# Performance work log

Measured on AMD Instinct MI355X. Metric: run time of the kernel, lower is better.

Reference implementation:

```python
import jax, jax.numpy as jnp
import numpy as np

N, E = 50000, 800000
IN, HID, H, C = 128, 64, 4, 2
NEG_SLOPE = 0.2


def _gat_layer(h, src, dst, W, al, ar, b, out_dim, residual, resW=None, act='elu'):
    # h: [N, in]; W: [H*out, in]; al/ar: [H, out]; b: [H*out]
    n = h.shape[0]
    feat = (h @ W.T).reshape(n, H, out_dim)            # [N, H, out]
    el = jnp.einsum('nho,ho->nh', feat, al)            # [N, H]
    er = jnp.einsum('nho,ho->nh', feat, ar)            # [N, H]
    e = jax.nn.leaky_relu(el[src] + er[dst], NEG_SLOPE)  # [E, H]
    # segment softmax over incoming edges of each dst node
    emax = jax.ops.segment_max(e, dst, num_segments=n)
    ee = jnp.exp(e - emax[dst])
    denom = jax.ops.segment_sum(ee, dst, num_segments=n)
    alpha = ee / denom[dst]                             # [E, H]
    msg = feat[src] * alpha[:, :, None]                 # [E, H, out]
    rst = jax.ops.segment_sum(msg, dst, num_segments=n)  # [N, H, out]
    if residual == 'id':
        rst = rst + h.reshape(n, H, out_dim)
    elif residual == 'fc':
        rst = rst + (h @ resW.T).reshape(n, H, out_dim)
    rst = rst + b.reshape(1, H, out_dim)
    if act == 'elu':
        rst = jax.nn.elu(rst)
    else:  # softmax over last dim (F.softmax)
        rst = jax.nn.softmax(rst, axis=-1)
    return rst


def setup_inputs() -> dict:
    key = jax.random.key(0)
    ks = jax.random.split(key, 24)
    x = jax.random.normal(ks[0], (N, IN), dtype=jnp.float32)
    src = jax.random.randint(ks[1], (E,), 0, N)
    dst = jax.random.randint(ks[2], (E,), 0, N)
    s = 0.1
    d = {'x': x, 'src': src, 'dst': dst}
    # layer 1: IN -> (H, HID), no residual
    d['W1'] = jax.random.normal(ks[3], (H * HID, IN), dtype=jnp.float32) * s
    d['al1'] = jax.random.normal(ks[4], (H, HID), dtype=jnp.float32) * s
    d['ar1'] = jax.random.normal(ks[5], (H, HID), dtype=jnp.float32) * s
    d['b1'] = jnp.zeros((H * HID,), dtype=jnp.float32)
    # layers 2,3: H*HID -> (H, HID), identity residual
    d['W2'] = jax.random.normal(ks[6], (H * HID, H * HID), dtype=jnp.float32) * s
    d['al2'] = jax.random.normal(ks[7], (H, HID), dtype=jnp.float32) * s
    d['ar2'] = jax.random.normal(ks[8], (H, HID), dtype=jnp.float32) * s
    d['b2'] = jnp.zeros((H * HID,), dtype=jnp.float32)
    d['W3'] = jax.random.normal(ks[9], (H * HID, H * HID), dtype=jnp.float32) * s
    d['al3'] = jax.random.normal(ks[10], (H, HID), dtype=jnp.float32) * s
    d['ar3'] = jax.random.normal(ks[11], (H, HID), dtype=jnp.float32) * s
    d['b3'] = jnp.zeros((H * HID,), dtype=jnp.float32)
    # layer 4: H*HID -> (H, C), linear residual, softmax activation, mean over heads
    d['W4'] = jax.random.normal(ks[12], (H * C, H * HID), dtype=jnp.float32) * s
    d['al4'] = jax.random.normal(ks[13], (H, C), dtype=jnp.float32) * s
    d['ar4'] = jax.random.normal(ks[14], (H, C), dtype=jnp.float32) * s
    d['b4'] = jnp.zeros((H * C,), dtype=jnp.float32)
    d['resW4'] = jax.random.normal(ks[15], (H * C, H * HID), dtype=jnp.float32) * s
    return d


def reference(x, src, dst, W1, al1, ar1, b1, W2, al2, ar2, b2, W3, al3, ar3, b3, W4, al4, ar4, b4, resW4):
    h = _gat_layer(x, src, dst, W1, al1, ar1, b1, HID, 'none', act='elu').reshape(N, H * HID)
    h = _gat_layer(h, src, dst, W2, al2, ar2, b2, HID, 'id', act='elu').reshape(N, H * HID)
    h = _gat_layer(h, src, dst, W3, al3, ar3, b3, HID, 'id', act='elu').reshape(N, H * HID)
    h = _gat_layer(h, src, dst, W4, al4, ar4, b4, C, 'fc', resW=resW4, act='softmax')
    return h.mean(axis=1)  # [N, C]
```

## Files before the change

### kernel.cpp

```cpp
#include <hip/hip_runtime.h>
#include <hip/hip_bf16.h>
#include <math.h>


#define LEAKY_SLOPE 0.2f

typedef __bf16 bf16x8_t __attribute__((ext_vector_type(8)));
typedef float f32x4_t __attribute__((ext_vector_type(4)));

__device__ __forceinline__ float leaky(float x) { return x > 0.f ? x : LEAKY_SLOPE * x; }
__device__ __forceinline__ float eluf(float x)  { return x > 0.f ? x : expm1f(x); }
__device__ __forceinline__ float bflo(unsigned u) { return __uint_as_float(u << 16); }
__device__ __forceinline__ float bfhi(unsigned u) { return __uint_as_float(u & 0xffff0000u); }

__device__ __forceinline__ int rli(int v, int l) { return __builtin_amdgcn_readlane(v, l); }
__device__ __forceinline__ float rlf(float v, int l) {
  return __uint_as_float((unsigned)__builtin_amdgcn_readlane((int)__float_as_uint(v), l));
}
template <int CTRL>
__device__ __forceinline__ float dpp_add(float x) {
  int t = __builtin_amdgcn_update_dpp(0, (int)__float_as_uint(x), CTRL, 0xf, 0xf, false);
  return x + __uint_as_float((unsigned)t);
}
__device__ __forceinline__ float wsum_dpp(float x) {
  x = dpp_add<0x111>(x);
  x = dpp_add<0x112>(x);
  x = dpp_add<0x114>(x);
  x = dpp_add<0x118>(x);
  x = dpp_add<0x142>(x);
  x = dpp_add<0x143>(x);
  return rlf(x, 63);
}
__device__ __forceinline__ float wmax(float v) {
#pragma unroll
  for (int o = 32; o; o >>= 1) v = fmaxf(v, __shfl_xor(v, o));
  return v;
}
__device__ __forceinline__ float wsum_sh(float v) {
#pragma unroll
  for (int o = 32; o; o >>= 1) v += __shfl_xor(v, o);
  return v;
}

__device__ __forceinline__ void gl_lds16(const __hip_bfloat16* g, __bf16* l) {
  __builtin_amdgcn_global_load_lds((const __attribute__((address_space(1))) void*)g,
                                   (__attribute__((address_space(3))) void*)l, 16, 0, 0);
}

__global__ void hist_k(const int* __restrict__ dst, int* __restrict__ deg, int e) {
  int i = blockIdx.x * 256 + threadIdx.x;
  if (i < e) atomicAdd(&deg[dst[i]], 1);
}

__global__ __launch_bounds__(1024) void scan1_k(const int* __restrict__ deg,
                                                int* __restrict__ rowp,
                                                int* __restrict__ bsum, int n) {
  __shared__ int sd[1024];
  int tid = threadIdx.x;
  int i = blockIdx.x * 1024 + tid;
  int v = (i < n) ? deg[i] : 0;
  int x = v;
  sd[tid] = x;
  __syncthreads();
  for (int off = 1; off < 1024; off <<= 1) {
    int t = (tid >= off) ? sd[tid - off] : 0;
    __syncthreads();
    x += t;
    sd[tid] = x;
    __syncthreads();
  }
  if (i < n) rowp[i] = x - v;
  if (tid == 1023) bsum[blockIdx.x] = x;
}

__global__ __launch_bounds__(64) void scan2_k(int* __restrict__ bsum, int nb) {
  int lane = threadIdx.x;
  if (nb <= 64) {
    int v = (lane < nb) ? bsum[lane] : 0;
    int x = v;
#pragma unroll
    for (int off = 1; off < 64; off <<= 1) {
      int t = __shfl_up(x, off);
      if (lane >= off) x += t;
    }
    if (lane < nb) bsum[lane] = x - v;
    if (lane == 63) bsum[nb] = x;
  } else if (lane == 0) {
    int run = 0;
    for (int i = 0; i < nb; ++i) { int t = bsum[i]; bsum[i] = run; run += t; }
    bsum[nb] = run;
  }
}

__global__ void scan3_k(const int* __restrict__ bsum, int* __restrict__ rowp, int n, int nb) {
  int i = blockIdx.x * 256 + threadIdx.x;
  if (i < n) rowp[i] += bsum[i >> 10];
  if (i == n) rowp[n] = bsum[nb];
}

__global__ void scatter_k(const int* __restrict__ src, const int* __restrict__ dst,
                          const int* __restrict__ rowp, int* __restrict__ cur,
                          int* __restrict__ csrc, int e) {
  int i = blockIdx.x * 256 + threadIdx.x;
  if (i < e) {
    int d = dst[i];
    int p = atomicAdd(&cur[d], 1);
    csrc[rowp[d] + p] = src[i];
  }
}

__global__ void cvtall_k(const float* __restrict__ x, const float* __restrict__ W1,
                         const float* __restrict__ W2, const float* __restrict__ W3,
                         const float* __restrict__ W4, const float* __restrict__ rW4,
                         __hip_bfloat16* __restrict__ xb, __hip_bfloat16* __restrict__ W1b,
                         __hip_bfloat16* __restrict__ W2b, __hip_bfloat16* __restrict__ W3b,
                         __hip_bfloat16* __restrict__ Wcatb, int nx) {
  int i = blockIdx.x * 256 + threadIdx.x;
  if (i < nx) { xb[i] = __float2bfloat16(x[i]); return; }
  int j = i - nx;
  if (j < 32768) W1b[j] = __float2bfloat16(W1[j]);
  else if (j < 98304)  { int k = j - 32768;  W2b[k] = __float2bfloat16(W2[k]); }
  else if (j < 163840) { int k = j - 98304;  W3b[k] = __float2bfloat16(W3[k]); }
  else if (j < 165888) { int k = j - 163840; Wcatb[k] = __float2bfloat16(W4[k]); }
  else if (j < 167936) { int k = j - 165888; Wcatb[2048 + k] = __float2bfloat16(rW4[k]); }
}

template <int K>
__global__ __launch_bounds__(256) void gemm_mfma(const __hip_bfloat16* __restrict__ A,
                                                 const __hip_bfloat16* __restrict__ B,
                                                 __hip_bfloat16* __restrict__ featb,
                                                 const float* __restrict__ al,
                                                 const float* __restrict__ ar,
                                                 float* __restrict__ el,
                                                 float* __restrict__ er, int n) {
  __shared__ __bf16 As[128 * 32];
  __shared__ __bf16 Bs[128 * 32];
  const int tid = threadIdx.x;
  const int lane = tid & 63, w = tid >> 6;
  const int tm = lane & 15, tq = lane >> 4;
  const int wm = (w & 1) * 64, wn = (w >> 1) * 64;
  const int r0 = blockIdx.x * 128, c0 = blockIdx.y * 128;

  f32x4_t acc[4][4];
#pragma unroll
  for (int i = 0; i < 4; ++i)
#pragma unroll
    for (int j = 0; j < 4; ++j) acc[i][j] = 0.f;

  const bool interior = (r0 + 128 <= n);
  if (interior) {
    const int srow = w * 32 + (lane >> 2);
    const int scol = (lane & 3) * 8;
    for (int kk = 0; kk < K; kk += 32) {
      __syncthreads();
      const __hip_bfloat16* ga = A + (size_t)(r0 + srow) * K + kk + scol;
      const __hip_bfloat16* gb = B + (size_t)(c0 + srow) * K + kk + scol;
      gl_lds16(ga, As + w * 1024);
      gl_lds16(ga + (size_t)16 * K, As + w * 1024 + 512);
      gl_lds16(gb, Bs + w * 1024);
      gl_lds16(gb + (size_t)16 * K, Bs + w * 1024 + 512);
      __syncthreads();
      bf16x8_t af[4], bfr[4];
#pragma unroll
      for (int i = 0; i < 4; ++i) af[i] = *(const bf16x8_t*)&As[(wm + i * 16 + tm) * 32 + tq * 8];
#pragma unroll
      for (int j = 0; j < 4; ++j) bfr[j] = *(const bf16x8_t*)&Bs[(wn + j * 16 + tm) * 32 + tq * 8];
#pragma unroll
      for (int i = 0; i < 4; ++i)
#pragma unroll
        for (int j = 0; j < 4; ++j)
          acc[i][j] = __builtin_amdgcn_mfma_f32_16x16x32_bf16(af[i], bfr[j], acc[i][j], 0, 0, 0);
    }
  } else {
    const int srow = tid >> 1, sko = (tid & 1) * 16;
    for (int kk = 0; kk < K; kk += 32) {
      uint4 av0 = {0, 0, 0, 0}, av1 = {0, 0, 0, 0};
      int arw = r0 + srow;
      if (arw < n) {
        const uint4* p = (const uint4*)(A + (size_t)arw * K + kk + sko);
        av0 = p[0];
        av1 = p[1];
      }
      const uint4* q = (const uint4*)(B + (size_t)(c0 + srow) * K + kk + sko);
      uint4 bv0 = q[0], bv1 = q[1];
      __syncthreads();
      *(uint4*)&As[srow * 32 + sko] = av0;
      *(uint4*)&As[srow * 32 + sko + 8] = av1;
      *(uint4*)&Bs[srow * 32 + sko] = bv0;
      *(uint4*)&Bs[srow * 32 + sko + 8] = bv1;
      __syncthreads();
      bf16x8_t af[4], bfr[4];
#pragma unroll
      for (int i = 0; i < 4; ++i) af[i] = *(const bf16x8_t*)&As[(wm + i * 16 + tm) * 32 + tq * 8];
#pragma unroll
      for (int j = 0; j < 4; ++j) bfr[j] = *(const bf16x8_t*)&Bs[(wn + j * 16 + tm) * 32 + tq * 8];
#pragma unroll
      for (int i = 0; i < 4; ++i)
#pragma unroll
        for (int j = 0; j < 4; ++j)
          acc[i][j] = __builtin_amdgcn_mfma_f32_16x16x32_bf16(af[i], bfr[j], acc[i][j], 0, 0, 0);
    }
  }

#pragma unroll
  for (int i = 0; i < 4; ++i) {
#pragma unroll
    for (int j = 0; j < 4; ++j) {
      int col = c0 + wn + j * 16 + tm;
      int hh = col >> 6, oo = col & 63;
#pragma unroll
      for (int rr = 0; rr < 4; ++rr) {
        int row = r0 + wm + i * 16 + tq * 4 + rr;
        if (row < n) featb[(size_t)row * 256 + oo * 4 + hh] = __float2bfloat16(acc[i][j][rr]);
      }
    }
  }

  {
    const int hd = (c0 + wn) >> 6;
    float alv[4], arv[4];
#pragma unroll
    for (int j = 0; j < 4; ++j) {
      alv[j] = al[hd * 64 + j * 16 + tm];
      arv[j] = ar[hd * 64 + j * 16 + tm];
    }
#pragma unroll
    for (int i = 0; i < 4; ++i) {
#pragma unroll
      for (int rr = 0; rr < 4; ++rr) {
        float se = acc[i][0][rr] * alv[0] + acc[i][1][rr] * alv[1] +
                   acc[i][2][rr] * alv[2] + acc[i][3][rr] * alv[3];
        float sr2 = acc[i][0][rr] * arv[0] + acc[i][1][rr] * arv[1] +
                    acc[i][2][rr] * arv[2] + acc[i][3][rr] * arv[3];
#pragma unroll
        for (int o = 1; o < 16; o <<= 1) {
          se += __shfl_xor(se, o);
          sr2 += __shfl_xor(sr2, o);
        }
        if (tm == 0) {
          int row = r0 + wm + i * 16 + tq * 4 + rr;
          if (row < n) {
            el[(size_t)row * 4 + hd] = se;
            er[(size_t)row * 4 + hd] = sr2;
          }
        }
      }
    }
  }
}

template <int RES>
__global__ __launch_bounds__(256) void agg64_k(const __hip_bfloat16* __restrict__ featb,
                                               const float* __restrict__ el,
                                               const float* __restrict__ er,
                                               const int* __restrict__ rowp,
                                               const int* __restrict__ csrc,
                                               const __hip_bfloat16* __restrict__ hinb,
                                               const float* __restrict__ bias,
                                               __hip_bfloat16* __restrict__ houtb, int n) {
  __shared__ float wsh[4][256];
  int wv = threadIdx.x >> 6;
  int node = blockIdx.x * 4 + wv;
  int lane = threadIdx.x & 63;
  if (node >= n) return;
  int s0 = rowp[node], s1 = rowp[node + 1];
  int deg = s1 - s0;
  float4 erv = *(const float4*)(er + (size_t)node * 4);
  float a0 = 0, a1 = 0, a2 = 0, a3 = 0;

  if (deg <= 64) {
    int sown = 0;
    float x0 = 0.f, x1 = 0.f, x2 = 0.f, x3 = 0.f;
    if (lane < deg) {
      sown = csrc[s0 + lane];
      float4 e = *(const float4*)(el + (size_t)sown * 4);
      x0 = __expf(leaky(e.x + erv.x));
      x1 = __expf(leaky(e.y + erv.y));
      x2 = __expf(leaky(e.z + erv.z));
      x3 = __expf(leaky(e.w + erv.w));
    }
    float d0 = wsum_dpp(x0), d1 = wsum_dpp(x1), d2 = wsum_dpp(x2), d3 = wsum_dpp(x3);
    float i0 = d0 > 0.f ? 1.f / d0 : 0.f;
    float i1 = d1 > 0.f ? 1.f / d1 : 0.f;
    float i2 = d2 > 0.f ? 1.f / d2 : 0.f;
    float i3 = d3 > 0.f ? 1.f / d3 : 0.f;
    float4 wq = {x0 * i0, x1 * i1, x2 * i2, x3 * i3};
    *(float4*)&wsh[wv][lane * 4] = wq;

    int k = 0;
    for (; k + 8 <= deg; k += 8) {
      int sk0 = rli(sown, k + 0), sk1 = rli(sown, k + 1);
      int sk2 = rli(sown, k + 2), sk3 = rli(sown, k + 3);
      int sk4 = rli(sown, k + 4), sk5 = rli(sown, k + 5);
      int sk6 = rli(sown, k + 6), sk7 = rli(sown, k + 7);
      uint2 u0 = ((const uint2*)(featb + ((size_t)sk0 << 8)))[lane];
      uint2 u1 = ((const uint2*)(featb + ((size_t)sk1 << 8)))[lane];
      uint2 u2 = ((const uint2*)(featb + ((size_t)sk2 << 8)))[lane];
      uint2 u3 = ((const uint2*)(featb + ((size_t)sk3 << 8)))[lane];
      uint2 u4 = ((const uint2*)(featb + ((size_t)sk4 << 8)))[lane];
      uint2 u5 = ((const uint2*)(featb + ((size_t)sk5 << 8)))[lane];
      uint2 u6 = ((const uint2*)(featb + ((size_t)sk6 << 8)))[lane];
      uint2 u7 = ((const uint2*)(featb + ((size_t)sk7 << 8)))[lane];
      float4 w0 = *(const float4*)&wsh[wv][(k + 0) * 4];
      float4 w1 = *(const float4*)&wsh[wv][(k + 1) * 4];
      float4 w2 = *(const float4*)&wsh[wv][(k + 2) * 4];
      float4 w3 = *(const float4*)&wsh[wv][(k + 3) * 4];
      float4 w4 = *(const float4*)&wsh[wv][(k + 4) * 4];
      float4 w5 = *(const float4*)&wsh[wv][(k + 5) * 4];
      float4 w6 = *(const float4*)&wsh[wv][(k + 6) * 4];
      float4 w7 = *(const float4*)&wsh[wv][(k + 7) * 4];
      a0 = fmaf(w0.x, bflo(u0.x), a0); a1 = fmaf(w0.y, bfhi(u0.x), a1);
      a2 = fmaf(w0.z, bflo(u0.y), a2); a3 = fmaf(w0.w, bfhi(u0.y), a3);
      a0 = fmaf(w1.x, bflo(u1.x), a0); a1 = fmaf(w1.y, bfhi(u1.x), a1);
      a2 = fmaf(w1.z, bflo(u1.y), a2); a3 = fmaf(w1.w, bfhi(u1.y), a3);
      a0 = fmaf(w2.x, bflo(u2.x), a0); a1 = fmaf(w2.y, bfhi(u2.x), a1);
      a2 = fmaf(w2.z, bflo(u2.y), a2); a3 = fmaf(w2.w, bfhi(u2.y), a3);
      a0 = fmaf(w3.x, bflo(u3.x), a0); a1 = fmaf(w3.y, bfhi(u3.x), a1);
      a2 = fmaf(w3.z, bflo(u3.y), a2); a3 = fmaf(w3.w, bfhi(u3.y), a3);
      a0 = fmaf(w4.x, bflo(u4.x), a0); a1 = fmaf(w4.y, bfhi(u4.x), a1);
      a2 = fmaf(w4.z, bflo(u4.y), a2); a3 = fmaf(w4.w, bfhi(u4.y), a3);
      a0 = fmaf(w5.x, bflo(u5.x), a0); a1 = fmaf(w5.y, bfhi(u5.x), a1);
      a2 = fmaf(w5.z, bflo(u5.y), a2); a3 = fmaf(w5.w, bfhi(u5.y), a3);
      a0 = fmaf(w6.x, bflo(u6.x), a0); a1 = fmaf(w6.y, bfhi(u6.x), a1);
      a2 = fmaf(w6.z, bflo(u6.y), a2); a3 = fmaf(w6.w, bfhi(u6.y), a3);
      a0 = fmaf(w7.x, bflo(u7.x), a0); a1 = fmaf(w7.y, bfhi(u7.x), a1);
      a2 = fmaf(w7.z, bflo(u7.y), a2); a3 = fmaf(w7.w, bfhi(u7.y), a3);
    }
    for (; k + 4 <= deg; k += 4) {
      int sk0 = rli(sown, k + 0), sk1 = rli(sown, k + 1);
      int sk2 = rli(sown, k + 2), sk3 = rli(sown, k + 3);
      uint2 u0 = ((const uint2*)(featb + ((size_t)sk0 << 8)))[lane];
      uint2 u1 = ((const uint2*)(featb + ((size_t)sk1 << 8)))[lane];
      uint2 u2 = ((const uint2*)(featb + ((size_t)sk2 << 8)))[lane];
      uint2 u3 = ((const uint2*)(featb + ((size_t)sk3 << 8)))[lane];
      float4 w0 = *(const float4*)&wsh[wv][(k + 0) * 4];
      float4 w1 = *(const float4*)&wsh[wv][(k + 1) * 4];
      float4 w2 = *(const float4*)&wsh[wv][(k + 2) * 4];
      float4 w3 = *(const float4*)&wsh[wv][(k + 3) * 4];
      a0 = fmaf(w0.x, bflo(u0.x), a0); a1 = fmaf(w0.y, bfhi(u0.x), a1);
      a2 = fmaf(w0.z, bflo(u0.y), a2); a3 = fmaf(w0.w, bfhi(u0.y), a3);
      a0 = fmaf(w1.x, bflo(u1.x), a0); a1 = fmaf(w1.y, bfhi(u1.x), a1);
      a2 = fmaf(w1.z, bflo(u1.y), a2); a3 = fmaf(w1.w, bfhi(u1.y), a3);
      a0 = fmaf(w2.x, bflo(u2.x), a0); a1 = fmaf(w2.y, bfhi(u2.x), a1);
      a2 = fmaf(w2.z, bflo(u2.y), a2); a3 = fmaf(w2.w, bfhi(u2.y), a3);
      a0 = fmaf(w3.x, bflo(u3.x), a0); a1 = fmaf(w3.y, bfhi(u3.x), a1);
      a2 = fmaf(w3.z, bflo(u3.y), a2); a3 = fmaf(w3.w, bfhi(u3.y), a3);
    }
    for (; k < deg; ++k) {
      int sk = rli(sown, k);
      uint2 u = ((const uint2*)(featb + ((size_t)sk << 8)))[lane];
      float4 wk = *(const float4*)&wsh[wv][k * 4];
      a0 = fmaf(wk.x, bflo(u.x), a0);
      a1 = fmaf(wk.y, bfhi(u.x), a1);
      a2 = fmaf(wk.z, bflo(u.y), a2);
      a3 = fmaf(wk.w, bfhi(u.y), a3);
    }
  } else {
    float m0 = -INFINITY, m1 = -INFINITY, m2 = -INFINITY, m3 = -INFINITY;
    for (int k = s0 + lane; k < s1; k += 64) {
      int s = csrc[k];
      float4 e = *(const float4*)(el + (size_t)s * 4);
      m0 = fmaxf(m0, leaky(e.x + erv.x));
      m1 = fmaxf(m1, leaky(e.y + erv.y));
      m2 = fmaxf(m2, leaky(e.z + erv.z));
      m3 = fmaxf(m3, leaky(e.w + erv.w));
    }
    m0 = wmax(m0); m1 = wmax(m1); m2 = wmax(m2); m3 = wmax(m3);
    float d0 = 0, d1 = 0, d2 = 0, d3 = 0;
    for (int k = s0 + lane; k < s1; k += 64) {
      int s = csrc[k];
      float4 e = *(const float4*)(el + (size_t)s * 4);
      d0 += __expf(leaky(e.x + erv.x) - m0);
      d1 += __expf(leaky(e.y + erv.y) - m1);
      d2 += __expf(leaky(e.z + erv.z) - m2);
      d3 += __expf(leaky(e.w + erv.w) - m3);
    }
    d0 = wsum_sh(d0); d1 = wsum_sh(d1); d2 = wsum_sh(d2); d3 = wsum_sh(d3);
    float j0 = d0 > 0.f ? 1.f / d0 : 0.f;
    float j1 = d1 > 0.f ? 1.f / d1 : 0.f;
    float j2 = d2 > 0.f ? 1.f / d2 : 0.f;
    float j3 = d3 > 0.f ? 1.f / d3 : 0.f;
    for (int k = s0; k < s1; ++k) {
      int s = csrc[k];
      float4 e = *(const float4*)(el + (size_t)s * 4);
      float w0 = __expf(leaky(e.x + erv.x) - m0) * j0;
      float w1 = __expf(leaky(e.y + erv.y) - m1) * j1;
      float w2 = __expf(leaky(e.z + erv.z) - m2) * j2;
      float w3 = __expf(leaky(e.w + erv.w) - m3) * j3;
      uint2 u = ((const uint2*)(featb + ((size_t)s << 8)))[lane];
      a0 = fmaf(w0, bflo(u.x), a0);
      a1 = fmaf(w1, bfhi(u.x), a1);
      a2 = fmaf(w2, bflo(u.y), a2);
      a3 = fmaf(w3, bfhi(u.y), a3);
    }
  }

  size_t base = (size_t)node * 256;
  float v0 = a0 + bias[lane];
  float v1 = a1 + bias[64 + lane];
  float v2 = a2 + bias[128 + lane];
  float v3 = a3 + bias[192 + lane];
  if (RES) {
    v0 += __bfloat162float(hinb[base + lane]);
    v1 += __bfloat162float(hinb[base + 64 + lane]);
    v2 += __bfloat162float(hinb[base + 128 + lane]);
    v3 += __bfloat162float(hinb[base + 192 + lane]);
  }
  houtb[base + lane]       = __float2bfloat16(eluf(v0));
  houtb[base + 64 + lane]  = __float2bfloat16(eluf(v1));
  houtb[base + 128 + lane] = __float2bfloat16(eluf(v2));
  houtb[base + 192 + lane] = __float2bfloat16(eluf(v3));
}

__global__ __launch_bounds__(256) void l4mfma_k(const __hip_bfloat16* __restrict__ hb,
                                                const __hip_bfloat16* __restrict__ Wcat,
                                                const float* __restrict__ al4,
                                                const float* __restrict__ ar4,
                                                float* __restrict__ feat4,
                                                float* __restrict__ res4,
                                                float* __restrict__ el4,
                                                float* __restrict__ er4, int n) {
  int wid = blockIdx.x * 4 + (threadIdx.x >> 6);
  int n16 = (n + 15) >> 4;
  if (wid >= n16) return;
  int lane = threadIdx.x & 63;
  int tm = lane & 15, tq = lane >> 4;
  int row = wid * 16 + tm;
  int rowc = row < n ? row : n - 1;
  const __hip_bfloat16* ap = hb + (size_t)rowc * 256 + tq * 8;
  const __hip_bfloat16* bp = Wcat + (size_t)tm * 256 + tq * 8;
  f32x4_t acc = {0.f, 0.f, 0.f, 0.f};
#pragma unroll
  for (int k = 0; k < 8; ++k) {
    bf16x8_t af = *(const bf16x8_t*)(ap + k * 32);
    bf16x8_t bf = *(const bf16x8_t*)(bp + k * 32);
    acc = __builtin_amdgcn_mfma_f32_16x16x32_bf16(af, bf, acc, 0, 0, 0);
  }
  float* dstp = (tm < 8) ? feat4 : res4;
  int cc = tm & 7;
  float a4 = (tm < 8) ? al4[tm] : 0.f;
  float r4 = (tm < 8) ? ar4[tm] : 0.f;
#pragma unroll
  for (int r = 0; r < 4; ++r) {
    int node = wid * 16 + tq * 4 + r;
    float te = acc[r] * a4;
    float tr = acc[r] * r4;
    te += __shfl_xor(te, 1);
    tr += __shfl_xor(tr, 1);
    if (node < n) {
      dstp[(size_t)node * 8 + cc] = acc[r];
      if (tm < 8 && (tm & 1) == 0) {
        el4[(size_t)node * 4 + (tm >> 1)] = te;
        er4[(size_t)node * 4 + (tm >> 1)] = tr;
      }
    }
  }
}

__global__ __launch_bounds__(256) void agg4_k(const float* __restrict__ feat4,
                                              const float* __restrict__ el4,
                                              const float* __restrict__ er4,
                                              const int* __restrict__ rowp,
                                              const int* __restrict__ csrc,
                                              const float* __restrict__ res4,
                                              const float* __restrict__ b4,
                                              float* __restrict__ out, int n) {
  __shared__ int ssh[4][64];
  __shared__ float wsh[4][256];
  int wv = threadIdx.x >> 6;
  int node = blockIdx.x * 4 + wv;
  int lane = threadIdx.x & 63;
  if (node >= n) return;
  int s0 = rowp[node], s1 = rowp[node + 1];
  int deg = s1 - s0;
  float4 erv = *(const float4*)(er4 + (size_t)node * 4);
  float acc = 0.f;
  float scale = 1.f;
  int p = lane & 7, hh = p >> 1;

  if (deg <= 64) {
    int sown = 0;
    float x0 = 0.f, x1 = 0.f, x2 = 0.f, x3 = 0.f;
    if (lane < deg) {
      sown = csrc[s0 + lane];
      float4 e = *(const float4*)(el4 + (size_t)sown * 4);
      x0 = __expf(leaky(e.x + erv.x));
      x1 = __expf(leaky(e.y + erv.y));
      x2 = __expf(leaky(e.z + erv.z));
      x3 = __expf(leaky(e.w + erv.w));
    }
    float d0 = wsum_dpp(x0), d1 = wsum_dpp(x1), d2 = wsum_dpp(x2), d3 = wsum_dpp(x3);
    float i0 = d0 > 0.f ? 1.f / d0 : 0.f;
    float i1 = d1 > 0.f ? 1.f / d1 : 0.f;
    float i2 = d2 > 0.f ? 1.f / d2 : 0.f;
    float i3 = d3 > 0.f ? 1.f / d3 : 0.f;
    scale = (hh == 0) ? i0 : (hh == 1) ? i1 : (hh == 2) ? i2 : i3;
    ssh[wv][lane] = sown;
    float4 wq = {x0, x1, x2, x3};
    *(float4*)&wsh[wv][lane * 4] = wq;
    int g = lane >> 3;
    int nt = (deg + 7) >> 3;
    for (int t = 0; t < nt; ++t) {
      int k = g + t * 8;
      bool ok = k < deg;
      int kk = k & 63;
      int sk = ssh[wv][kk];
      float wk = wsh[wv][kk * 4 + hh];
      if (ok) acc = fmaf(wk, feat4[(size_t)sk * 8 + p], acc);
    }
    acc += __shfl_xor(acc, 8);
    acc += __shfl_xor(acc, 16);
    acc += __shfl_xor(acc, 32);
  } else {
    float m0 = -INFINITY, m1 = -INFINITY, m2 = -INFINITY, m3 = -INFINITY;
    for (int k = s0 + lane; k < s1; k += 64) {
      int s = csrc[k];
      float4 e = *(const float4*)(el4 + (size_t)s * 4);
      m0 = fmaxf(m0, leaky(e.x + erv.x));
      m1 = fmaxf(m1, leaky(e.y + erv.y));
      m2 = fmaxf(m2, leaky(e.z + erv.z));
      m3 = fmaxf(m3, leaky(e.w + erv.w));
    }
    m0 = wmax(m0); m1 = wmax(m1); m2 = wmax(m2); m3 = wmax(m3);
    float d0 = 0, d1 = 0, d2 = 0, d3 = 0;
    for (int k = s0 + lane; k < s1; k += 64) {
      int s = csrc[k];
      float4 e = *(const float4*)(el4 + (size_t)s * 4);
      d0 += __expf(leaky(e.x + erv.x) - m0);
      d1 += __expf(leaky(e.y + erv.y) - m1);
      d2 += __expf(leaky(e.z + erv.z) - m2);
      d3 += __expf(leaky(e.w + erv.w) - m3);
    }
    d0 = wsum_sh(d0); d1 = wsum_sh(d1); d2 = wsum_sh(d2); d3 = wsum_sh(d3);
    float i0 = d0 > 0.f ? 1.f / d0 : 0.f;
    float i1 = d1 > 0.f ? 1.f / d1 : 0.f;
    float i2 = d2 > 0.f ? 1.f / d2 : 0.f;
    float i3 = d3 > 0.f ? 1.f / d3 : 0.f;
    for (int k = s0; k < s1; ++k) {
      int s = csrc[k];
      float4 e = *(const float4*)(el4 + (size_t)s * 4);
      float w0 = __expf(leaky(e.x + erv.x) - m0) * i0;
      float w1 = __expf(leaky(e.y + erv.y) - m1) * i1;
      float w2 = __expf(leaky(e.z + erv.z) - m2) * i2;
      float w3 = __expf(leaky(e.w + erv.w) - m3) * i3;
      float wk = (hh == 0) ? w0 : (hh == 1) ? w1 : (hh == 2) ? w2 : w3;
      if (lane < 8) acc = fmaf(wk, feat4[(size_t)s * 8 + p], acc);
    }
  }

  float v = 0.f;
  if (lane < 8) v = acc * scale + res4[(size_t)node * 8 + lane] + b4[lane];
  float pv = __shfl_xor(v, 1);
  float mx = fmaxf(v, pv);
  float ex = __expf(v - mx);
  float sm = ex + __shfl_xor(ex, 1);
  float pr = ex / sm;
  float t = pr + __shfl_xor(pr, 2);
  t += __shfl_xor(t, 4);
  if (lane < 2) out[(size_t)node * 2 + lane] = t * 0.25f;
}

extern "C" void kernel_launch(void* const* d_in, const int* in_sizes, int n_in,
                              void* d_out, int out_size, void* d_ws, size_t ws_size,
                              hipStream_t stream) {
  const float* x   = (const float*)d_in[0];
  const int* src   = (const int*)d_in[1];
  const int* dst   = (const int*)d_in[2];
  const float* W1  = (const float*)d_in[3];
  const float* al1 = (const float*)d_in[4];
  const float* ar1 = (const float*)d_in[5];
  const float* b1  = (const float*)d_in[6];
  const float* W2  = (const float*)d_in[7];
  const float* al2 = (const float*)d_in[8];
  const float* ar2 = (const float*)d_in[9];
  const float* b2  = (const float*)d_in[10];
  const float* W3  = (const float*)d_in[11];
  const float* al3 = (const float*)d_in[12];
  const float* ar3 = (const float*)d_in[13];
  const float* b3  = (const float*)d_in[14];
  const float* W4  = (const float*)d_in[15];
  const float* al4 = (const float*)d_in[16];
  const float* ar4 = (const float*)d_in[17];
  const float* b4  = (const float*)d_in[18];
  const float* rW4 = (const float*)d_in[19];
  float* out = (float*)d_out;

  const int n = in_sizes[0] / 128;
  const int e = in_sizes[1];

  char* ws = (char*)d_ws;
  auto alloc = [&](size_t bytes) -> char* {
    char* p = ws;
    ws += (bytes + 255) & ~(size_t)255;
    return p;
  };
  __hip_bfloat16* featb = (__hip_bfloat16*)alloc((size_t)n * 256 * 2);
  __hip_bfloat16* h1b   = (__hip_bfloat16*)alloc((size_t)n * 256 * 2);
  __hip_bfloat16* h2b   = (__hip_bfloat16*)alloc((size_t)n * 256 * 2);
  __hip_bfloat16* h3b   = (__hip_bfloat16*)alloc((size_t)n * 256 * 2);
  __hip_bfloat16* xb    = (__hip_bfloat16*)alloc((size_t)n * 128 * 2);
  __hip_bfloat16* W1b   = (__hip_bfloat16*)alloc((size_t)256 * 128 * 2);
  __hip_bfloat16* W2b   = (__hip_bfloat16*)alloc((size_t)256 * 256 * 2);
  __hip_bfloat16* W3b   = (__hip_bfloat16*)alloc((size_t)256 * 256 * 2);
  __hip_bfloat16* Wcatb = (__hip_bfloat16*)alloc((size_t)16 * 256 * 2);
  float* el    = (float*)alloc((size_t)n * 4 * 4);
  float* er    = (float*)alloc((size_t)n * 4 * 4);
  float* feat4 = (float*)alloc((size_t)n * 8 * 4);
  float* res4  = (float*)alloc((size_t)n * 8 * 4);
  float* el4   = (float*)alloc((size_t)n * 4 * 4);
  float* er4   = (float*)alloc((size_t)n * 4 * 4);
  int* deg     = (int*)alloc((size_t)n * 4);
  int* cur     = (int*)alloc((size_t)n * 4);
  int* rowp    = (int*)alloc((size_t)(n + 1) * 4);
  int* csrc    = (int*)alloc((size_t)e * 4);
  int nb_scan  = (n + 1023) / 1024;
  int* bsum    = (int*)alloc((size_t)(nb_scan + 1) * 4);

  (void)hipMemsetAsync(deg, 0, (size_t)n * 4, stream);
  (void)hipMemsetAsync(cur, 0, (size_t)n * 4, stream);
  hist_k<<<(e + 255) / 256, 256, 0, stream>>>(dst, deg, e);
  scan1_k<<<nb_scan, 1024, 0, stream>>>(deg, rowp, bsum, n);
  scan2_k<<<1, 64, 0, stream>>>(bsum, nb_scan);
  scan3_k<<<(n + 256) / 256, 256, 0, stream>>>(bsum, rowp, n, nb_scan);
  scatter_k<<<(e + 255) / 256, 256, 0, stream>>>(src, dst, rowp, cur, csrc, e);

  int nx = n * 128;
  cvtall_k<<<(nx + 167936 + 255) / 256, 256, 0, stream>>>(x, W1, W2, W3, W4, rW4, xb, W1b,
                                                          W2b, W3b, Wcatb, nx);

  dim3 ggrid((n + 127) / 128, 2);
  int nb4 = (n + 3) / 4;

  gemm_mfma<128><<<ggrid, 256, 0, stream>>>(xb, W1b, featb, al1, ar1, el, er, n);
  agg64_k<0><<<nb4, 256, 0, stream>>>(featb, el, er, rowp, csrc, nullptr, b1, h1b, n);
  gemm_mfma<256><<<ggrid, 256, 0, stream>>>(h1b, W2b, featb, al2, ar2, el, er, n);
  agg64_k<1><<<nb4, 256, 0, stream>>>(featb, el, er, rowp, csrc, h1b, b2, h2b, n);
  gemm_mfma<256><<<ggrid, 256, 0, stream>>>(h2b, W3b, featb, al3, ar3, el, er, n);
  agg64_k<1><<<nb4, 256, 0, stream>>>(featb, el, er, rowp, csrc, h2b, b3, h3b, n);
  int n16 = (n + 15) / 16;
  l4mfma_k<<<(n16 + 3) / 4, 256, 0, stream>>>(h3b, Wcatb, al4, ar4, feat4, res4, el4, er4, n);
  agg4_k<<<nb4, 256, 0, stream>>>(feat4, el4, er4, rowp, csrc, res4, b4, out, n);
}
```

Before: 508.7 us.

## Fuse histogram into conversion, merge scan passes, use DPP and packed FMA

Folds the degree histogram into the bf16 conversion kernel and merges the second and third scan stages into one kernel, cutting launches and a memset. The GEMM epilogue row reduction switches from shuffles to DPP row shifts, writing from lane 15. The aggregation accumulators use packed 2-wide FMA. The merged scan now assumes at most 64 scan blocks, dropping the serial fallback.

```diff
diff --git a/kernel.cpp b/kernel.cpp
--- a/kernel.cpp
+++ b/kernel.cpp
@@ -7,6 +7,7 @@
 
 typedef __bf16 bf16x8_t __attribute__((ext_vector_type(8)));
 typedef float f32x4_t __attribute__((ext_vector_type(4)));
+typedef float f32x2_t __attribute__((ext_vector_type(2)));
 
 __device__ __forceinline__ float leaky(float x) { return x > 0.f ? x : LEAKY_SLOPE * x; }
 __device__ __forceinline__ float eluf(float x)  { return x > 0.f ? x : expm1f(x); }
@@ -31,6 +32,13 @@
   x = dpp_add<0x143>(x);
   return rlf(x, 63);
 }
+__device__ __forceinline__ float rowsum_dpp(float x) {
+  x = dpp_add<0x111>(x);
+  x = dpp_add<0x112>(x);
+  x = dpp_add<0x114>(x);
+  x = dpp_add<0x118>(x);
+  return x;
+}
 __device__ __forceinline__ float wmax(float v) {
 #pragma unroll
   for (int o = 32; o; o >>= 1) v = fmaxf(v, __shfl_xor(v, o));
@@ -40,16 +48,20 @@
 #pragma unroll
   for (int o = 32; o; o >>= 1) v += __shfl_xor(v, o);
   return v;
+}
+
+__device__ __forceinline__ void edge_fma(f32x2_t& a01, f32x2_t& a23, uint2 u, float4 w) {
+  f32x2_t f01 = {bflo(u.x), bfhi(u.x)};
+  f32x2_t f23 = {bflo(u.y), bfhi(u.y)};
+  f32x2_t w01 = {w.x, w.y};
+  f32x2_t w23 = {w.z, w.w};
+  a01 = __builtin_elementwise_fma(w01, f01, a01);
+  a23 = __builtin_elementwise_fma(w23, f23, a23);
 }
 
 __device__ __forceinline__ void gl_lds16(const __hip_bfloat16* g, __bf16* l) {
   __builtin_amdgcn_global_load_lds((const __attribute__((address_space(1))) void*)g,
                                    (__attribute__((address_space(3))) void*)l, 16, 0, 0);
-}
-
-__global__ void hist_k(const int* __restrict__ dst, int* __restrict__ deg, int e) {
-  int i = blockIdx.x * 256 + threadIdx.x;
-  if (i < e) atomicAdd(&deg[dst[i]], 1);
 }
 
 __global__ __launch_bounds__(1024) void scan1_k(const int* __restrict__ deg,
@@ -73,29 +85,24 @@
   if (tid == 1023) bsum[blockIdx.x] = x;
 }
 
-__global__ __launch_bounds__(64) void scan2_k(int* __restrict__ bsum, int nb) {
-  int lane = threadIdx.x;
-  if (nb <= 64) {
-    int v = (lane < nb) ? bsum[lane] : 0;
+__global__ void scan23_k(const int* __restrict__ bsum, int* __restrict__ rowp, int n, int nb) {
+  __shared__ int pref[65];
+  int tid = threadIdx.x;
+  if (tid < 64) {
+    int v = (tid < nb) ? bsum[tid] : 0;
     int x = v;
 #pragma unroll
     for (int off = 1; off < 64; off <<= 1) {
       int t = __shfl_up(x, off);
-      if (lane >= off) x += t;
-    }
-    if (lane < nb) bsum[lane] = x - v;
-    if (lane == 63) bsum[nb] = x;
-  } else if (lane == 0) {
-    int run = 0;
-    for (int i = 0; i < nb; ++i) { int t = bsum[i]; bsum[i] = run; run += t; }
-    bsum[nb] = run;
-  }
-}
-
-__global__ void scan3_k(const int* __restrict__ bsum, int* __restrict__ rowp, int n, int nb) {
-  int i = blockIdx.x * 256 + threadIdx.x;
-  if (i < n) rowp[i] += bsum[i >> 10];
-  if (i == n) rowp[n] = bsum[nb];
+      if (tid >= off) x += t;
+    }
+    pref[tid] = x - v;
+    if (tid == 63) pref[64] = x;
+  }
+  __syncthreads();
+  int i = blockIdx.x * 256 + tid;
+  if (i < n) rowp[i] += pref[i >> 10];
+  if (i == n) rowp[n] = pref[64];
 }
 
 __global__ void scatter_k(const int* __restrict__ src, const int* __restrict__ dst,
@@ -109,13 +116,15 @@
   }
 }
 
-__global__ void cvtall_k(const float* __restrict__ x, const float* __restrict__ W1,
-                         const float* __restrict__ W2, const float* __restrict__ W3,
-                         const float* __restrict__ W4, const float* __restrict__ rW4,
-                         __hip_bfloat16* __restrict__ xb, __hip_bfloat16* __restrict__ W1b,
-                         __hip_bfloat16* __restrict__ W2b, __hip_bfloat16* __restrict__ W3b,
-                         __hip_bfloat16* __restrict__ Wcatb, int nx) {
+__global__ void cvthist_k(const float* __restrict__ x, const float* __restrict__ W1,
+                          const float* __restrict__ W2, const float* __restrict__ W3,
+                          const float* __restrict__ W4, const float* __restrict__ rW4,
+                          __hip_bfloat16* __restrict__ xb, __hip_bfloat16* __restrict__ W1b,
+                          __hip_bfloat16* __restrict__ W2b, __hip_bfloat16* __restrict__ W3b,
+                          __hip_bfloat16* __restrict__ Wcatb, int nx,
+                          const int* __restrict__ dst, int* __restrict__ deg, int e) {
   int i = blockIdx.x * 256 + threadIdx.x;
+  if (i < e) atomicAdd(&deg[dst[i]], 1);
   if (i < nx) { xb[i] = __float2bfloat16(x[i]); return; }
   int j = i - nx;
   if (j < 32768) W1b[j] = __float2bfloat16(W1[j]);
@@ -232,12 +241,9 @@
                    acc[i][2][rr] * alv[2] + acc[i][3][rr] * alv[3];
         float sr2 = acc[i][0][rr] * arv[0] + acc[i][1][rr] * arv[1] +
                     acc[i][2][rr] * arv[2] + acc[i][3][rr] * arv[3];
-#pragma unroll
-        for (int o = 1; o < 16; o <<= 1) {
-          se += __shfl_xor(se, o);
-          sr2 += __shfl_xor(sr2, o);
-        }
-        if (tm == 0) {
+        se = rowsum_dpp(se);
+        sr2 = rowsum_dpp(sr2);
+        if (tm == 15) {
           int row = r0 + wm + i * 16 + tq * 4 + rr;
           if (row < n) {
             el[(size_t)row * 4 + hd] = se;
@@ -266,7 +272,7 @@
   int s0 = rowp[node], s1 = rowp[node + 1];
   int deg = s1 - s0;
   float4 erv = *(const float4*)(er + (size_t)node * 4);
-  float a0 = 0, a1 = 0, a2 = 0, a3 = 0;
+  f32x2_t a01 = {0.f, 0.f}, a23 = {0.f, 0.f};
 
   if (deg <= 64) {
     int sown = 0;
@@ -301,30 +307,14 @@
       uint2 u5 = ((const uint2*)(featb + ((size_t)sk5 << 8)))[lane];
       uint2 u6 = ((const uint2*)(featb + ((size_t)sk6 << 8)))[lane];
       uint2 u7 = ((const uint2*)(featb + ((size_t)sk7 << 8)))[lane];
-      float4 w0 = *(const float4*)&wsh[wv][(k + 0) * 4];
-      float4 w1 = *(const float4*)&wsh[wv][(k + 1) * 4];
-      float4 w2 = *(const float4*)&wsh[wv][(k + 2) * 4];
-      float4 w3 = *(const float4*)&wsh[wv][(k + 3) * 4];
-      float4 w4 = *(const float4*)&wsh[wv][(k + 4) * 4];
-      float4 w5 = *(const float4*)&wsh[wv][(k + 5) * 4];
-      float4 w6 = *(const float4*)&wsh[wv][(k + 6) * 4];
-      float4 w7 = *(const float4*)&wsh[wv][(k + 7) * 4];
-      a0 = fmaf(w0.x, bflo(u0.x), a0); a1 = fmaf(w0.y, bfhi(u0.x), a1);
-      a2 = fmaf(w0.z, bflo(u0.y), a2); a3 = fmaf(w0.w, bfhi(u0.y), a3);
-      a0 = fmaf(w1.x, bflo(u1.x), a0); a1 = fmaf(w1.y, bfhi(u1.x), a1);
-      a2 = fmaf(w1.z, bflo(u1.y), a2); a3 = fmaf(w1.w, bfhi(u1.y), a3);
-      a0 = fmaf(w2.x, bflo(u2.x), a0); a1 = fmaf(w2.y, bfhi(u2.x), a1);
-      a2 = fmaf(w2.z, bflo(u2.y), a2); a3 = fmaf(w2.w, bfhi(u2.y), a3);
-      a0 = fmaf(w3.x, bflo(u3.x), a0); a1 = fmaf(w3.y, bfhi(u3.x), a1);
-      a2 = fmaf(w3.z, bflo(u3.y), a2); a3 = fmaf(w3.w, bfhi(u3.y), a3);
-      a0 = fmaf(w4.x, bflo(u4.x), a0); a1 = fmaf(w4.y, bfhi(u4.x), a1);
-      a2 = fmaf(w4.z, bflo(u4.y), a2); a3 = fmaf(w4.w, bfhi(u4.y), a3);
-      a0 = fmaf(w5.x, bflo(u5.x), a0); a1 = fmaf(w5.y, bfhi(u5.x), a1);
-      a2 = fmaf(w5.z, bflo(u5.y), a2); a3 = fmaf(w5.w, bfhi(u5.y), a3);
-      a0 = fmaf(w6.x, bflo(u6.x), a0); a1 = fmaf(w6.y, bfhi(u6.x), a1);
-      a2 = fmaf(w6.z, bflo(u6.y), a2); a3 = fmaf(w6.w, bfhi(u6.y), a3);
-      a0 = fmaf(w7.x, bflo(u7.x), a0); a1 = fmaf(w7.y, bfhi(u7.x), a1);
-      a2 = fmaf(w7.z, bflo(u7.y), a2); a3 = fmaf(w7.w, bfhi(u7.y), a3);
+      edge_fma(a01, a23, u0, *(const float4*)&wsh[wv][(k + 0) * 4]);
+      edge_fma(a01, a23, u1, *(const float4*)&wsh[wv][(k + 1) * 4]);
+      edge_fma(a01, a23, u2, *(const float4*)&wsh[wv][(k + 2) * 4]);
+      edge_fma(a01, a23, u3, *(const float4*)&wsh[wv][(k + 3) * 4]);
+      edge_fma(a01, a23, u4, *(const float4*)&wsh[wv][(k + 4) * 4]);
+      edge_fma(a01, a23, u5, *(const float4*)&wsh[wv][(k + 5) * 4]);
+      edge_fma(a01, a23, u6, *(const float4*)&wsh[wv][(k + 6) * 4]);
+      edge_fma(a01, a23, u7, *(const float4*)&wsh[wv][(k + 7) * 4]);
     }
     for (; k + 4 <= deg; k += 4) {
       int sk0 = rli(sown, k + 0), sk1 = rli(sown, k + 1);
@@ -333,27 +323,15 @@
       uint2 u1 = ((const uint2*)(featb + ((size_t)sk1 << 8)))[lane];
       uint2 u2 = ((const uint2*)(featb + ((size_t)sk2 << 8)))[lane];
       uint2 u3 = ((const uint2*)(featb + ((size_t)sk3 << 8)))[lane];
-      float4 w0 = *(const float4*)&wsh[wv][(k + 0) * 4];
-      float4 w1 = *(const float4*)&wsh[wv][(k + 1) * 4];
-      float4 w2 = *(const float4*)&wsh[wv][(k + 2) * 4];
-      float4 w3 = *(const float4*)&wsh[wv][(k + 3) * 4];
-      a0 = fmaf(w0.x, bflo(u0.x), a0); a1 = fmaf(w0.y, bfhi(u0.x), a1);
-      a2 = fmaf(w0.z, bflo(u0.y), a2); a3 = fmaf(w0.w, bfhi(u0.y), a3);
-      a0 = fmaf(w1.x, bflo(u1.x), a0); a1 = fmaf(w1.y, bfhi(u1.x), a1);
-      a2 = fmaf(w1.z, bflo(u1.y), a2); a3 = fmaf(w1.w, bfhi(u1.y), a3);
-      a0 = fmaf(w2.x, bflo(u2.x), a0); a1 = fmaf(w2.y, bfhi(u2.x), a1);
-      a2 = fmaf(w2.z, bflo(u2.y), a2); a3 = fmaf(w2.w, bfhi(u2.y), a3);
-      a0 = fmaf(w3.x, bflo(u3.x), a0); a1 = fmaf(w3.y, bfhi(u3.x), a1);
-      a2 = fmaf(w3.z, bflo(u3.y), a2); a3 = fmaf(w3.w, bfhi(u3.y), a3);
+      edge_fma(a01, a23, u0, *(const float4*)&wsh[wv][(k + 0) * 4]);
+      edge_fma(a01, a23, u1, *(const float4*)&wsh[wv][(k + 1) * 4]);
+      edge_fma(a01, a23, u2, *(const float4*)&wsh[wv][(k + 2) * 4]);
+      edge_fma(a01, a23, u3, *(const float4*)&wsh[wv][(k + 3) * 4]);
     }
     for (; k < deg; ++k) {
       int sk = rli(sown, k);
       uint2 u = ((const uint2*)(featb + ((size_t)sk << 8)))[lane];
-      float4 wk = *(const float4*)&wsh[wv][k * 4];
-      a0 = fmaf(wk.x, bflo(u.x), a0);
-      a1 = fmaf(wk.y, bfhi(u.x), a1);
-      a2 = fmaf(wk.z, bflo(u.y), a2);
-      a3 = fmaf(wk.w, bfhi(u.y), a3);
+      edge_fma(a01, a23, u, *(const float4*)&wsh[wv][k * 4]);
     }
   } else {
     float m0 = -INFINITY, m1 = -INFINITY, m2 = -INFINITY, m3 = -INFINITY;
@@ -383,23 +361,21 @@
     for (int k = s0; k < s1; ++k) {
       int s = csrc[k];
       float4 e = *(const float4*)(el + (size_t)s * 4);
-      float w0 = __expf(leaky(e.x + erv.x) - m0) * j0;
-      float w1 = __expf(leaky(e.y + erv.y) - m1) * j1;
-      float w2 = __expf(leaky(e.z + erv.z) - m2) * j2;
-      float w3 = __expf(leaky(e.w + erv.w) - m3) * j3;
+      float4 wk;
+      wk.x = __expf(leaky(e.x + erv.x) - m0) * j0;
+      wk.y = __expf(leaky(e.y + erv.y) - m1) * j1;
+      wk.z = __expf(leaky(e.z + erv.z) - m2) * j2;
+      wk.w = __expf(leaky(e.w + erv.w) - m3) * j3;
       uint2 u = ((const uint2*)(featb + ((size_t)s << 8)))[lane];
-      a0 = fmaf(w0, bflo(u.x), a0);
-      a1 = fmaf(w1, bfhi(u.x), a1);
-      a2 = fmaf(w2, bflo(u.y), a2);
-      a3 = fmaf(w3, bfhi(u.y), a3);
+      edge_fma(a01, a23, u, wk);
     }
   }
 
   size_t base = (size_t)node * 256;
-  float v0 = a0 + bias[lane];
-  float v1 = a1 + bias[64 + lane];
-  float v2 = a2 + bias[128 + lane];
-  float v3 = a3 + bias[192 + lane];
+  float v0 = a01[0] + bias[lane];
+  float v1 = a01[1] + bias[64 + lane];
+  float v2 = a23[0] + bias[128 + lane];
+  float v3 = a23[1] + bias[192 + lane];
   if (RES) {
     v0 += __bfloat162float(hinb[base + lane]);
     v1 += __bfloat162float(hinb[base + 64 + lane]);
@@ -609,24 +585,21 @@
   float* res4  = (float*)alloc((size_t)n * 8 * 4);
   float* el4   = (float*)alloc((size_t)n * 4 * 4);
   float* er4   = (float*)alloc((size_t)n * 4 * 4);
-  int* deg     = (int*)alloc((size_t)n * 4);
-  int* cur     = (int*)alloc((size_t)n * 4);
+  int* deg     = (int*)alloc((size_t)2 * n * 4);
+  int* cur     = deg + n;
   int* rowp    = (int*)alloc((size_t)(n + 1) * 4);
   int* csrc    = (int*)alloc((size_t)e * 4);
   int nb_scan  = (n + 1023) / 1024;
   int* bsum    = (int*)alloc((size_t)(nb_scan + 1) * 4);
 
-  (void)hipMemsetAsync(deg, 0, (size_t)n * 4, stream);
-  (void)hipMemsetAsync(cur, 0, (size_t)n * 4, stream);
-  hist_k<<<(e + 255) / 256, 256, 0, stream>>>(dst, deg, e);
+  (void)hipMemsetAsync(deg, 0, (size_t)2 * n * 4, stream);
+
+  int nx = n * 128;
+  cvthist_k<<<(nx + 167936 + 255) / 256, 256, 0, stream>>>(x, W1, W2, W3, W4, rW4, xb, W1b,
+                                                           W2b, W3b, Wcatb, nx, dst, deg, e);
   scan1_k<<<nb_scan, 1024, 0, stream>>>(deg, rowp, bsum, n);
-  scan2_k<<<1, 64, 0, stream>>>(bsum, nb_scan);
-  scan3_k<<<(n + 256) / 256, 256, 0, stream>>>(bsum, rowp, n, nb_scan);
+  scan23_k<<<(n + 256) / 256, 256, 0, stream>>>(bsum, rowp, n, nb_scan);
   scatter_k<<<(e + 255) / 256, 256, 0, stream>>>(src, dst, rowp, cur, csrc, e);
-
-  int nx = n * 128;
-  cvtall_k<<<(nx + 167936 + 255) / 256, 256, 0, stream>>>(x, W1, W2, W3, W4, rW4, xb, W1b,
-                                                          W2b, W3b, Wcatb, nx);
 
   dim3 ggrid((n + 127) / 128, 2);
   int nb4 = (n + 3) / 4;
```

Result: no change. 498.8 us (-1.9%).
